# Kernel tuning notes

Measured on AMD Instinct MI355X. Metric: run time of the kernel, lower is better.

## Reference

```python
import jax, jax.numpy as jnp
import numpy as np

B, S, D, M, H, HD, V = 256, 128, 512, 150, 8, 64, 10000
LN_EPS = 1e-5

def layer_norm(x, g, b):
    mu = jnp.mean(x, axis=-1, keepdims=True)
    var = jnp.mean((x - mu) ** 2, axis=-1, keepdims=True)
    return (x - mu) * jax.lax.rsqrt(var + LN_EPS) * g + b

def setup_inputs() -> dict:
    key = jax.random.key(0)
    ks = jax.random.split(key, 20)
    s = 0.02
    return {
        'x': jax.random.randint(ks[0], (B, S), 0, V),
        'emb': jax.random.normal(ks[1], (V, D)) * s,
        'W1': jax.random.normal(ks[2], (M, D, D)) * s,   # [mode, out, in]
        'b1': jnp.zeros((M, D)),
        'ln1_g': jnp.ones((M, D)),
        'ln1_b': jnp.zeros((M, D)),
        'W2': jax.random.normal(ks[3], (M, D, D)) * s,
        'b2': jnp.zeros((M, D)),
        'dbias': jax.random.normal(ks[4], (M, D)) * 0.01,
        'in_proj_w': jax.random.normal(ks[5], (3 * D, D)) * s,
        'in_proj_b': jnp.zeros((3 * D,)),
        'out_proj_w': jax.random.normal(ks[6], (D, D)) * s,
        'out_proj_b': jnp.zeros((D,)),
        'norm_g': jnp.ones((D,)),
        'norm_b': jnp.zeros((D,)),
        'dec_w1': jax.random.normal(ks[7], (D // 2, D)) * s,
        'dec_b1': jnp.zeros((D // 2,)),
        'dec_w2': jax.random.normal(ks[8], (V, D // 2)) * s,
        'dec_b2': jnp.zeros((V,)),
    }

def reference(x, emb, W1, b1, ln1_g, ln1_b, W2, b2, dbias,
              in_proj_w, in_proj_b, out_proj_w, out_proj_b,
              norm_g, norm_b, dec_w1, dec_b1, dec_w2, dec_b2):
    # shared embedding: [B,S] -> [B,D]
    e = jnp.take(emb, x, axis=0).mean(axis=1)
    # 150 mode heads as grouped GEMMs: Linear -> LN -> ReLU -> Linear + bias
    h = jnp.einsum('bd,mod->bmo', e, W1) + b1                    # [B,M,D]
    h = layer_norm(h, ln1_g, ln1_b)
    h = jax.nn.relu(h)                                            # dropout = identity (eval)
    mode_out = jnp.einsum('bmd,mod->bmo', h, W2) + b2 + dbias     # [B,M,D]
    # cross-mode self-attention (torch MultiheadAttention, batch_first)
    qkv = mode_out @ in_proj_w.T + in_proj_b                      # [B,M,3D]
    q, k, v = jnp.split(qkv, 3, axis=-1)
    q = q.reshape(B, M, H, HD); k = k.reshape(B, M, H, HD); v = v.reshape(B, M, H, HD)
    scores = jnp.einsum('bqhd,bkhd->bhqk', q, k) / np.sqrt(HD)
    attn = jax.nn.softmax(scores, axis=-1)
    o = jnp.einsum('bhqk,bkhd->bqhd', attn, v).reshape(B, M, D)
    attended = o @ out_proj_w.T + out_proj_b                      # [B,M,D]
    # gating mask: active_modes=None -> all ones, so gated == attended
    agg = layer_norm(attended.sum(axis=1), norm_g, norm_b)        # [B,D]
    # decoder: Linear -> ReLU -> Linear
    dec = jax.nn.relu(agg @ dec_w1.T + dec_b1)
    return dec @ dec_w2.T + dec_b2                                # [B,V]
```

## Files before the change

kernel.cpp:

```cpp
#include <hip/hip_runtime.h>

typedef __attribute__((ext_vector_type(8))) short s16x8;
typedef __attribute__((ext_vector_type(8))) unsigned short u16x8;
typedef __attribute__((ext_vector_type(4))) float f32x4;

#define LN_EPS 1e-5f

__device__ inline float bf2f(unsigned short u) {
    union { unsigned int i; float f; } x; x.i = ((unsigned int)u) << 16; return x.f;
}
__device__ inline unsigned short f2bf(float f) {
    unsigned int u = __builtin_bit_cast(unsigned int, f);
    u += 0x7FFFu + ((u >> 16) & 1u);
    return (unsigned short)(u >> 16);
}
__device__ inline unsigned int cvt_pk_bf16(float lo, float hi) {
    unsigned int r;
    asm("v_cvt_pk_bf16_f32 %0, %1, %2" : "=v"(r) : "v"(lo), "v"(hi));
    return r;
}
typedef __attribute__((address_space(1))) const unsigned int as1_u32;
typedef __attribute__((address_space(3))) unsigned int as3_u32;
__device__ inline void gl2lds16(const void* g, void* l) {
    __builtin_amdgcn_global_load_lds((as1_u32*)g, (as3_u32*)l, 16, 0, 0);
}

template<int K, bool RELU, bool F32OUT>
__global__ __launch_bounds__(256, 3) void gemm_k32_kernel(
    const unsigned short* __restrict__ A,
    const float* __restrict__ W,
    const float* __restrict__ bias1,
    const float* __restrict__ bias2,
    float bias_scale,
    void* __restrict__ Cv,
    int N, int gx, int gy,
    size_t strideA_mode, size_t lda,
    size_t strideW_mode, size_t strideB_mode,
    size_t strideC_mode, size_t ldc)
{
    constexpr int NSTEP = K / 32;

    const int nwg = gridDim.x, wgid = blockIdx.x;
    const int q8 = nwg >> 3, r8 = nwg & 7;
    const int xcd = wgid & 7, sub = wgid >> 3;
    int p = (xcd < r8 ? xcd * (q8 + 1) : r8 * (q8 + 1) + (xcd - r8) * q8) + sub;
    const int bx = p % gx; p /= gx;
    const int by = p % gy;
    const int bz = p / gy;
    const int n0 = bx * 128, r0 = by * 128;

    __shared__ __align__(16) unsigned char lds[2][24576];

    const int tid = threadIdx.x, lane = tid & 63, wid = tid >> 6;
    const int fr = lane & 15, ks = lane >> 4;
    const int wr = (wid >> 1) * 64, wc = (wid & 1) * 64;

    const int Ia0 = (wid * 2 + 0) * 64 + lane;
    const int Ia1 = (wid * 2 + 1) * 64 + lane;
    const int ar0 = Ia0 >> 2, ac0 = (Ia0 & 3) ^ (ar0 & 3);
    const int ar1 = Ia1 >> 2, ac1 = (Ia1 & 3) ^ (ar1 & 3);
    const unsigned char* Aslab = (const unsigned char*)(A + (size_t)bz * strideA_mode);
    const unsigned char* aSrc0 = Aslab + (size_t)(r0 + ar0) * lda * 2 + ac0 * 16;
    const unsigned char* aSrc1 = Aslab + (size_t)(r0 + ar1) * lda * 2 + ac1 * 16;

    const unsigned char* Wslab = (const unsigned char*)(W + (size_t)bz * strideW_mode);
    const unsigned char* bSrc[4];
#pragma unroll
    for (int j = 0; j < 4; ++j) {
        const int I = (wid * 4 + j) * 64 + lane;
        const int brow = I >> 3, bcp = I & 7;
        const int bcl = bcp ^ (brow & 7);
        const int growb = min(n0 + brow, N - 1);
        bSrc[j] = Wslab + (size_t)growb * K * 4 + bcl * 16;
    }

    f32x4 acc[4][4];
#pragma unroll
    for (int i = 0; i < 4; ++i)
#pragma unroll
        for (int j = 0; j < 4; ++j)
#pragma unroll
            for (int r = 0; r < 4; ++r) acc[i][j][r] = 0.f;

    auto stage = [&](int buf, int t) {
        gl2lds16(aSrc0 + (size_t)t * 64, &lds[buf][(wid * 2 + 0) * 1024]);
        gl2lds16(aSrc1 + (size_t)t * 64, &lds[buf][(wid * 2 + 1) * 1024]);
#pragma unroll
        for (int j = 0; j < 4; ++j)
            gl2lds16(bSrc[j] + (size_t)t * 128, &lds[buf][8192 + (wid * 4 + j) * 1024]);
    };

    auto compute = [&](int buf) {
        const unsigned char* Ab = &lds[buf][0];
        const unsigned char* Bb = &lds[buf][8192];
        s16x8 af[4];
#pragma unroll
        for (int mi = 0; mi < 4; ++mi)
            af[mi] = *(const s16x8*)(Ab + (wr + mi * 16 + fr) * 64 + ((ks ^ (fr & 3)) << 4));
        s16x8 bfr[4];
#pragma unroll
        for (int ni = 0; ni < 4; ++ni) {
            const int brow = wc + ni * 16 + fr;
            const float4 v0 = *(const float4*)(Bb + brow * 128 + (((2 * ks + 0) ^ (fr & 7)) << 4));
            const float4 v1 = *(const float4*)(Bb + brow * 128 + (((2 * ks + 1) ^ (fr & 7)) << 4));
            union { unsigned int u[4]; s16x8 s; } r;
            r.u[0] = cvt_pk_bf16(v0.x, v0.y);
            r.u[1] = cvt_pk_bf16(v0.z, v0.w);
            r.u[2] = cvt_pk_bf16(v1.x, v1.y);
            r.u[3] = cvt_pk_bf16(v1.z, v1.w);
            bfr[ni] = r.s;
        }
#pragma unroll
        for (int mi = 0; mi < 4; ++mi)
#pragma unroll
            for (int ni = 0; ni < 4; ++ni)
                acc[mi][ni] = __builtin_amdgcn_mfma_f32_16x16x32_bf16(af[mi], bfr[ni], acc[mi][ni], 0, 0, 0);
    };

    stage(0, 0);
    __syncthreads();

    for (int t = 0; t < NSTEP; t += 2) {
        stage(1, t + 1);
        compute(0);
        __syncthreads();
        if (t + 2 < NSTEP) stage(0, t + 2);
        compute(1);
        __syncthreads();
    }

    if (!F32OUT) {
        unsigned short* Cl = (unsigned short*)&lds[0][0];
#pragma unroll
        for (int ni = 0; ni < 4; ++ni) {
            const int col = n0 + wc + ni * 16 + fr;
            float bsum = 0.f;
            if (bias1) bsum += bias_scale * bias1[(size_t)bz * strideB_mode + col];
            if (bias2) bsum += bias2[(size_t)bz * strideB_mode + col];
#pragma unroll
            for (int mi = 0; mi < 4; ++mi)
#pragma unroll
                for (int r = 0; r < 4; ++r) {
                    float v = acc[mi][ni][r] + bsum;
                    if (RELU) v = fmaxf(v, 0.f);
                    Cl[(wr + mi * 16 + ks * 4 + r) * 128 + wc + ni * 16 + fr] = f2bf(v);
                }
        }
        __syncthreads();
        unsigned short* Cg = (unsigned short*)Cv + (size_t)bz * strideC_mode;
#pragma unroll
        for (int it = 0; it < 8; ++it) {
            const int c = it * 256 + tid;
            const int row = c >> 4, ch = c & 15;
            u16x8 v = *(const u16x8*)(&Cl[row * 128 + ch * 8]);
            *(u16x8*)(Cg + (size_t)(r0 + row) * ldc + n0 + ch * 8) = v;
        }
    } else {
#pragma unroll
        for (int ni = 0; ni < 4; ++ni) {
            const int col = n0 + wc + ni * 16 + fr;
            if (col < N) {
                float bsum = 0.f;
                if (bias1) bsum += bias_scale * bias1[(size_t)bz * strideB_mode + col];
                if (bias2) bsum += bias2[(size_t)bz * strideB_mode + col];
#pragma unroll
                for (int mi = 0; mi < 4; ++mi)
#pragma unroll
                    for (int r = 0; r < 4; ++r) {
                        const int row = r0 + wr + mi * 16 + ks * 4 + r;
                        float v = acc[mi][ni][r] + bsum;
                        if (RELU) v = fmaxf(v, 0.f);
                        ((float*)Cv)[(size_t)bz * strideC_mode + (size_t)row * ldc + col] = v;
                    }
            }
        }
    }
}

__global__ __launch_bounds__(512) void embed_kernel(
    const int* __restrict__ x, const float* __restrict__ emb,
    unsigned short* __restrict__ e)
{
    const int b = blockIdx.x;
    __shared__ int xs[128];
    const int tid = threadIdx.x;
    if (tid < 128) xs[tid] = x[b * 128 + tid];
    __syncthreads();
    float s = 0.f;
    for (int i = 0; i < 128; ++i) s += emb[(size_t)xs[i] * 512 + tid];
    e[(size_t)b * 512 + tid] = f2bf(s * (1.f / 128.f));
}

template<bool RELU>
__global__ __launch_bounds__(256) void ln_kernel(
    const unsigned short* __restrict__ X,
    const float* __restrict__ G,
    const float* __restrict__ Bt,
    unsigned short* __restrict__ Y,
    int M)
{
    const int row = blockIdx.x;
    const int m = row % M;
    const unsigned short* xr = X + (size_t)row * 512;
    unsigned short* yr = Y + (size_t)row * 512;
    const int tid = threadIdx.x;
    const float x0 = bf2f(xr[tid]), x1 = bf2f(xr[tid + 256]);
    float s = x0 + x1, q = x0 * x0 + x1 * x1;
#pragma unroll
    for (int off = 32; off; off >>= 1) {
        s += __shfl_xor(s, off);
        q += __shfl_xor(q, off);
    }
    __shared__ float red[4][2];
    const int wid = tid >> 6, lane = tid & 63;
    if (lane == 0) { red[wid][0] = s; red[wid][1] = q; }
    __syncthreads();
    s = red[0][0] + red[1][0] + red[2][0] + red[3][0];
    q = red[0][1] + red[1][1] + red[2][1] + red[3][1];
    const float mu = s * (1.f / 512.f);
    const float var = q * (1.f / 512.f) - mu * mu;
    const float rstd = rsqrtf(var + LN_EPS);
    const float* g = G + (size_t)m * 512;
    const float* bt = Bt + (size_t)m * 512;
    float y0 = (x0 - mu) * rstd * g[tid] + bt[tid];
    float y1 = (x1 - mu) * rstd * g[tid + 256] + bt[tid + 256];
    if (RELU) { y0 = fmaxf(y0, 0.f); y1 = fmaxf(y1, 0.f); }
    yr[tid] = f2bf(y0);
    yr[tid + 256] = f2bf(y1);
}

#define KP 72
#define VP 168
__global__ __launch_bounds__(256) void attn_mfma_kernel(
    const unsigned short* __restrict__ qkv, unsigned short* __restrict__ o_att)
{
    const int b = blockIdx.x >> 3, h = blockIdx.x & 7;
    __shared__ __align__(16) unsigned short k_s[160 * KP];
    __shared__ __align__(16) unsigned short v_t[64 * VP];
    __shared__ __align__(16) unsigned short p_s[4][16 * VP];
    const int tid = threadIdx.x, lane = tid & 63, wid = tid >> 6;
    const int fr = lane & 15, ks = lane >> 4;
    const size_t base = (size_t)b * (150 * 1536) + h * 64;

    for (int idx = tid; idx < 160 * 8; idx += 256) {
        const int r = idx >> 3, c8 = (idx & 7) * 8;
        u16x8 v;
        if (r < 150) v = *(const u16x8*)(qkv + base + (size_t)r * 1536 + 512 + c8);
        else {
#pragma unroll
            for (int j = 0; j < 8; ++j) v[j] = 0;
        }
        *(u16x8*)(&k_s[r * KP + c8]) = v;
    }
    for (int idx = tid; idx < 160 * 8; idx += 256) {
        const int c8 = idx / 160, r = idx - c8 * 160;
        u16x8 v;
        if (r < 150) v = *(const u16x8*)(qkv + base + (size_t)r * 1536 + 1024 + c8 * 8);
        else {
#pragma unroll
            for (int j = 0; j < 8; ++j) v[j] = 0;
        }
#pragma unroll
        for (int j = 0; j < 8; ++j) v_t[(c8 * 8 + j) * VP + r] = v[j];
    }
    __syncthreads();

    unsigned short* pw = &p_s[wid][0];

    for (int qt = wid; qt < 10; qt += 4) {
        const int qr = (qt * 16 + fr < 150) ? qt * 16 + fr : 149;
        const unsigned short* qp = qkv + base + (size_t)qr * 1536;
        s16x8 qa0 = *(const s16x8*)(qp + ks * 8);
        s16x8 qa1 = *(const s16x8*)(qp + 32 + ks * 8);

        f32x4 acc[10];
#pragma unroll
        for (int t = 0; t < 10; ++t)
#pragma unroll
            for (int r = 0; r < 4; ++r) acc[t][r] = 0.f;
#pragma unroll
        for (int t = 0; t < 10; ++t) {
            s16x8 kb0 = *(const s16x8*)(&k_s[(t * 16 + fr) * KP + ks * 8]);
            s16x8 kb1 = *(const s16x8*)(&k_s[(t * 16 + fr) * KP + 32 + ks * 8]);
            acc[t] = __builtin_amdgcn_mfma_f32_16x16x32_bf16(qa0, kb0, acc[t], 0, 0, 0);
            acc[t] = __builtin_amdgcn_mfma_f32_16x16x32_bf16(qa1, kb1, acc[t], 0, 0, 0);
        }

        const bool v9 = (fr < 6);
        float inv[4];
#pragma unroll
        for (int i = 0; i < 4; ++i) {
            float m = -1e30f;
#pragma unroll
            for (int t = 0; t < 9; ++t) m = fmaxf(m, acc[t][i]);
            if (v9) m = fmaxf(m, acc[9][i]);
#pragma unroll
            for (int off = 1; off < 16; off <<= 1) m = fmaxf(m, __shfl_xor(m, off));
            float s = 0.f;
#pragma unroll
            for (int t = 0; t < 10; ++t) {
                float e = 0.f;
                if (t < 9 || v9) e = __expf(0.125f * (acc[t][i] - m));
                s += e;
                pw[(ks * 4 + i) * VP + t * 16 + fr] = f2bf(e);
            }
#pragma unroll
            for (int off = 1; off < 16; off <<= 1) s += __shfl_xor(s, off);
            inv[i] = 1.f / s;
        }

        f32x4 o[4];
#pragma unroll
        for (int dt = 0; dt < 4; ++dt)
#pragma unroll
            for (int r = 0; r < 4; ++r) o[dt][r] = 0.f;
#pragma unroll
        for (int kc = 0; kc < 5; ++kc) {
            s16x8 pa = *(const s16x8*)(&pw[fr * VP + kc * 32 + ks * 8]);
#pragma unroll
            for (int dt = 0; dt < 4; ++dt) {
                s16x8 vb = *(const s16x8*)(&v_t[(dt * 16 + fr) * VP + kc * 32 + ks * 8]);
                o[dt] = __builtin_amdgcn_mfma_f32_16x16x32_bf16(pa, vb, o[dt], 0, 0, 0);
            }
        }

#pragma unroll
        for (int dt = 0; dt < 4; ++dt) {
            const int d = h * 64 + dt * 16 + fr;
#pragma unroll
            for (int i = 0; i < 4; ++i) {
                const int q = qt * 16 + ks * 4 + i;
                if (q < 150)
                    o_att[((size_t)(b * 150 + q)) * 512 + d] = f2bf(o[dt][i] * inv[i]);
            }
        }
    }
}

__global__ __launch_bounds__(512) void osum_kernel(
    const unsigned short* __restrict__ o_att, unsigned short* __restrict__ osum)
{
    const int b = blockIdx.x, tid = threadIdx.x;
    float s = 0.f;
    const unsigned short* p = o_att + (size_t)b * 150 * 512 + tid;
    for (int mm = 0; mm < 150; ++mm) s += bf2f(p[(size_t)mm * 512]);
    osum[(size_t)b * 512 + tid] = f2bf(s);
}

extern "C" void kernel_launch(void* const* d_in, const int* in_sizes, int n_in,
                              void* d_out, int out_size, void* d_ws, size_t ws_size,
                              hipStream_t stream)
{
    (void)in_sizes; (void)n_in; (void)out_size; (void)ws_size;

    const int*   x          = (const int*)d_in[0];
    const float* emb        = (const float*)d_in[1];
    const float* W1         = (const float*)d_in[2];
    const float* b1         = (const float*)d_in[3];
    const float* ln1_g      = (const float*)d_in[4];
    const float* ln1_b      = (const float*)d_in[5];
    const float* W2         = (const float*)d_in[6];
    const float* b2         = (const float*)d_in[7];
    const float* dbias      = (const float*)d_in[8];
    const float* in_proj_w  = (const float*)d_in[9];
    const float* in_proj_b  = (const float*)d_in[10];
    const float* out_proj_w = (const float*)d_in[11];
    const float* out_proj_b = (const float*)d_in[12];
    const float* norm_g     = (const float*)d_in[13];
    const float* norm_b     = (const float*)d_in[14];
    const float* dec_w1     = (const float*)d_in[15];
    const float* dec_b1     = (const float*)d_in[16];
    const float* dec_w2     = (const float*)d_in[17];
    const float* dec_b2     = (const float*)d_in[18];

    char* ws = (char*)d_ws;
    unsigned short* e_bf  = (unsigned short*)(ws + 0x0);
    unsigned short* osum  = (unsigned short*)(ws + 0x40000);
    unsigned short* att1  = (unsigned short*)(ws + 0x80000);
    unsigned short* agg   = (unsigned short*)(ws + 0xC0000);
    unsigned short* dec1  = (unsigned short*)(ws + 0x100000);
    unsigned short* h1    = (unsigned short*)(ws + 0x200000);
    unsigned short* mo    = (unsigned short*)(ws + 0x2800000);
    unsigned short* qkvf  = (unsigned short*)(ws + 0x4E00000);
    unsigned short* o_att = h1;

    embed_kernel<<<256, 512, 0, stream>>>(x, emb, e_bf);

    gemm_k32_kernel<512, false, false><<<4 * 2 * 150, 256, 0, stream>>>(
        e_bf, W1, b1, nullptr, 1.f, h1,
        512, 4, 2,
        (size_t)0, 512, (size_t)512 * 512, 512, 512, 76800);

    ln_kernel<true><<<38400, 256, 0, stream>>>(h1, ln1_g, ln1_b, h1, 150);

    gemm_k32_kernel<512, false, false><<<4 * 2 * 150, 256, 0, stream>>>(
        h1, W2, b2, dbias, 1.f, mo,
        512, 4, 2,
        (size_t)512, 76800, (size_t)512 * 512, 512, 512, 76800);

    gemm_k32_kernel<512, false, false><<<12 * 300, 256, 0, stream>>>(
        mo, in_proj_w, in_proj_b, nullptr, 1.f, qkvf,
        1536, 12, 300,
        (size_t)0, 512, (size_t)0, 0, 0, 1536);

    attn_mfma_kernel<<<2048, 256, 0, stream>>>(qkvf, o_att);

    osum_kernel<<<256, 512, 0, stream>>>(o_att, osum);

    gemm_k32_kernel<512, false, false><<<4 * 2, 256, 0, stream>>>(
        osum, out_proj_w, out_proj_b, nullptr, 150.f, att1,
        512, 4, 2,
        (size_t)0, 512, (size_t)0, 0, 0, 512);

    ln_kernel<false><<<256, 256, 0, stream>>>(att1, norm_g, norm_b, agg, 1);

    gemm_k32_kernel<512, true, false><<<2 * 2, 256, 0, stream>>>(
        agg, dec_w1, dec_b1, nullptr, 1.f, dec1,
        256, 2, 2,
        (size_t)0, 512, (size_t)0, 0, 0, 256);

    gemm_k32_kernel<256, false, true><<<79 * 2, 256, 0, stream>>>(
        dec1, dec_w2, dec_b2, nullptr, 1.f, d_out,
        10000, 79, 2,
        (size_t)0, 256, (size_t)0, 0, 0, 10000);
}
```

Measured before the change: 407.4 us.

## Pre-convert weights to bf16 and chunk QKV GEMM with attention per batch slice

Adds a conversion kernel that turns every fp32 weight matrix into bf16 in the workspace before use. The GEMM kernel now streams bf16 weights, which halves weight traffic and LDS per stage, removes the in-loop fp32-to-bf16 conversions and allows occupancy 4. Separately, the QKV projection and attention now run in four batch chunks of 64 so the QKV buffer stays small and likely cache-resident. The trade-off is an extra full read and write pass over the 150-mode W1/W2 weights on every call, plus more kernel launches.

```diff
diff --git a/kernel.cpp b/kernel.cpp
--- a/kernel.cpp
+++ b/kernel.cpp
@@ -25,10 +25,27 @@
     __builtin_amdgcn_global_load_lds((as1_u32*)g, (as3_u32*)l, 16, 0, 0);
 }
 
+__global__ __launch_bounds__(256) void cvt_bf16_kernel(
+    const float* __restrict__ in, unsigned short* __restrict__ out, int n8)
+{
+    int i = blockIdx.x * 256 + threadIdx.x;
+    const int stride = gridDim.x * 256;
+    for (; i < n8; i += stride) {
+        const float4 a = ((const float4*)in)[2 * i];
+        const float4 b = ((const float4*)in)[2 * i + 1];
+        union { unsigned int u[4]; u16x8 v; } r;
+        r.u[0] = cvt_pk_bf16(a.x, a.y);
+        r.u[1] = cvt_pk_bf16(a.z, a.w);
+        r.u[2] = cvt_pk_bf16(b.x, b.y);
+        r.u[3] = cvt_pk_bf16(b.z, b.w);
+        ((u16x8*)out)[i] = r.v;
+    }
+}
+
 template<int K, bool RELU, bool F32OUT>
-__global__ __launch_bounds__(256, 3) void gemm_k32_kernel(
+__global__ __launch_bounds__(256, 4) void gemm_bf_kernel(
     const unsigned short* __restrict__ A,
-    const float* __restrict__ W,
+    const unsigned short* __restrict__ Wb,
     const float* __restrict__ bias1,
     const float* __restrict__ bias2,
     float bias_scale,
@@ -49,7 +66,7 @@
     const int bz = p / gy;
     const int n0 = bx * 128, r0 = by * 128;
 
-    __shared__ __align__(16) unsigned char lds[2][24576];
+    __shared__ __align__(16) unsigned char lds[2][16384];
 
     const int tid = threadIdx.x, lane = tid & 63, wid = tid >> 6;
     const int fr = lane & 15, ks = lane >> 4;
@@ -62,17 +79,10 @@
     const unsigned char* Aslab = (const unsigned char*)(A + (size_t)bz * strideA_mode);
     const unsigned char* aSrc0 = Aslab + (size_t)(r0 + ar0) * lda * 2 + ac0 * 16;
     const unsigned char* aSrc1 = Aslab + (size_t)(r0 + ar1) * lda * 2 + ac1 * 16;
-
-    const unsigned char* Wslab = (const unsigned char*)(W + (size_t)bz * strideW_mode);
-    const unsigned char* bSrc[4];
-#pragma unroll
-    for (int j = 0; j < 4; ++j) {
-        const int I = (wid * 4 + j) * 64 + lane;
-        const int brow = I >> 3, bcp = I & 7;
-        const int bcl = bcp ^ (brow & 7);
-        const int growb = min(n0 + brow, N - 1);
-        bSrc[j] = Wslab + (size_t)growb * K * 4 + bcl * 16;
-    }
+    const unsigned char* Wslab = (const unsigned char*)(Wb + (size_t)bz * strideW_mode);
+    const int br0 = min(n0 + ar0, N - 1), br1 = min(n0 + ar1, N - 1);
+    const unsigned char* bSrc0 = Wslab + (size_t)br0 * K * 2 + ac0 * 16;
+    const unsigned char* bSrc1 = Wslab + (size_t)br1 * K * 2 + ac1 * 16;
 
     f32x4 acc[4][4];
 #pragma unroll
@@ -85,31 +95,21 @@
     auto stage = [&](int buf, int t) {
         gl2lds16(aSrc0 + (size_t)t * 64, &lds[buf][(wid * 2 + 0) * 1024]);
         gl2lds16(aSrc1 + (size_t)t * 64, &lds[buf][(wid * 2 + 1) * 1024]);
-#pragma unroll
-        for (int j = 0; j < 4; ++j)
-            gl2lds16(bSrc[j] + (size_t)t * 128, &lds[buf][8192 + (wid * 4 + j) * 1024]);
+        gl2lds16(bSrc0 + (size_t)t * 64, &lds[buf][8192 + (wid * 2 + 0) * 1024]);
+        gl2lds16(bSrc1 + (size_t)t * 64, &lds[buf][8192 + (wid * 2 + 1) * 1024]);
     };
 
     auto compute = [&](int buf) {
         const unsigned char* Ab = &lds[buf][0];
         const unsigned char* Bb = &lds[buf][8192];
-        s16x8 af[4];
+        const int co = (ks ^ (fr & 3)) << 4;
+        s16x8 af[4], bfr[4];
 #pragma unroll
         for (int mi = 0; mi < 4; ++mi)
-            af[mi] = *(const s16x8*)(Ab + (wr + mi * 16 + fr) * 64 + ((ks ^ (fr & 3)) << 4));
-        s16x8 bfr[4];
-#pragma unroll
-        for (int ni = 0; ni < 4; ++ni) {
-            const int brow = wc + ni * 16 + fr;
-            const float4 v0 = *(const float4*)(Bb + brow * 128 + (((2 * ks + 0) ^ (fr & 7)) << 4));
-            const float4 v1 = *(const float4*)(Bb + brow * 128 + (((2 * ks + 1) ^ (fr & 7)) << 4));
-            union { unsigned int u[4]; s16x8 s; } r;
-            r.u[0] = cvt_pk_bf16(v0.x, v0.y);
-            r.u[1] = cvt_pk_bf16(v0.z, v0.w);
-            r.u[2] = cvt_pk_bf16(v1.x, v1.y);
-            r.u[3] = cvt_pk_bf16(v1.z, v1.w);
-            bfr[ni] = r.s;
-        }
+            af[mi] = *(const s16x8*)(Ab + (wr + mi * 16 + fr) * 64 + co);
+#pragma unroll
+        for (int ni = 0; ni < 4; ++ni)
+            bfr[ni] = *(const s16x8*)(Bb + (wc + ni * 16 + fr) * 64 + co);
 #pragma unroll
         for (int mi = 0; mi < 4; ++mi)
 #pragma unroll
@@ -232,15 +232,16 @@
 #define KP 72
 #define VP 168
 __global__ __launch_bounds__(256) void attn_mfma_kernel(
-    const unsigned short* __restrict__ qkv, unsigned short* __restrict__ o_att)
-{
-    const int b = blockIdx.x >> 3, h = blockIdx.x & 7;
+    const unsigned short* __restrict__ qkv, unsigned short* __restrict__ o_att,
+    int b0)
+{
+    const int bl = blockIdx.x >> 3, h = blockIdx.x & 7;
     __shared__ __align__(16) unsigned short k_s[160 * KP];
     __shared__ __align__(16) unsigned short v_t[64 * VP];
     __shared__ __align__(16) unsigned short p_s[4][16 * VP];
     const int tid = threadIdx.x, lane = tid & 63, wid = tid >> 6;
     const int fr = lane & 15, ks = lane >> 4;
-    const size_t base = (size_t)b * (150 * 1536) + h * 64;
+    const size_t base = (size_t)bl * (150 * 1536) + h * 64;
 
     for (int idx = tid; idx < 160 * 8; idx += 256) {
         const int r = idx >> 3, c8 = (idx & 7) * 8;
@@ -331,7 +332,7 @@
             for (int i = 0; i < 4; ++i) {
                 const int q = qt * 16 + ks * 4 + i;
                 if (q < 150)
-                    o_att[((size_t)(b * 150 + q)) * 512 + d] = f2bf(o[dt][i] * inv[i]);
+                    o_att[((size_t)((b0 + bl) * 150 + q)) * 512 + d] = f2bf(o[dt][i] * inv[i]);
             }
         }
     }
@@ -381,46 +382,61 @@
     unsigned short* dec1  = (unsigned short*)(ws + 0x100000);
     unsigned short* h1    = (unsigned short*)(ws + 0x200000);
     unsigned short* mo    = (unsigned short*)(ws + 0x2800000);
-    unsigned short* qkvf  = (unsigned short*)(ws + 0x4E00000);
+    unsigned short* qkvb  = (unsigned short*)(ws + 0x4E00000);
+    unsigned short* Wbf   = (unsigned short*)(ws + 0x6B00000);
+    unsigned short* ipwbf = (unsigned short*)(ws + 0xB600000);
+    unsigned short* opwbf = (unsigned short*)(ws + 0xB780000);
+    unsigned short* dw1bf = (unsigned short*)(ws + 0xB800000);
+    unsigned short* dw2bf = (unsigned short*)(ws + 0xB840000);
     unsigned short* o_att = h1;
 
     embed_kernel<<<256, 512, 0, stream>>>(x, emb, e_bf);
 
-    gemm_k32_kernel<512, false, false><<<4 * 2 * 150, 256, 0, stream>>>(
-        e_bf, W1, b1, nullptr, 1.f, h1,
+    cvt_bf16_kernel<<<384, 256, 0, stream>>>(in_proj_w, ipwbf, 1536 * 512 / 8);
+    cvt_bf16_kernel<<<128, 256, 0, stream>>>(out_proj_w, opwbf, 512 * 512 / 8);
+    cvt_bf16_kernel<<<64, 256, 0, stream>>>(dec_w1, dw1bf, 256 * 512 / 8);
+    cvt_bf16_kernel<<<1280, 256, 0, stream>>>(dec_w2, dw2bf, 10000 * 256 / 8);
+
+    cvt_bf16_kernel<<<2048, 256, 0, stream>>>(W1, Wbf, 150 * 512 * 512 / 8);
+
+    gemm_bf_kernel<512, false, false><<<4 * 2 * 150, 256, 0, stream>>>(
+        e_bf, Wbf, b1, nullptr, 1.f, h1,
         512, 4, 2,
         (size_t)0, 512, (size_t)512 * 512, 512, 512, 76800);
 
     ln_kernel<true><<<38400, 256, 0, stream>>>(h1, ln1_g, ln1_b, h1, 150);
 
-    gemm_k32_kernel<512, false, false><<<4 * 2 * 150, 256, 0, stream>>>(
-        h1, W2, b2, dbias, 1.f, mo,
+    cvt_bf16_kernel<<<2048, 256, 0, stream>>>(W2, Wbf, 150 * 512 * 512 / 8);
+
+    gemm_bf_kernel<512, false, false><<<4 * 2 * 150, 256, 0, stream>>>(
+        h1, Wbf, b2, dbias, 1.f, mo,
         512, 4, 2,
         (size_t)512, 76800, (size_t)512 * 512, 512, 512, 76800);
 
-    gemm_k32_kernel<512, false, false><<<12 * 300, 256, 0, stream>>>(
-        mo, in_proj_w, in_proj_b, nullptr, 1.f, qkvf,
-        1536, 12, 300,
-        (size_t)0, 512, (size_t)0, 0, 0, 1536);
-
-    attn_mfma_kernel<<<2048, 256, 0, stream>>>(qkvf, o_att);
+    for (int c = 0; c < 4; ++c) {
+        gemm_bf_kernel<512, false, false><<<12 * 75, 256, 0, stream>>>(
+            mo + (size_t)c * 64 * 76800, ipwbf, in_proj_b, nullptr, 1.f, qkvb,
+            1536, 12, 75,
+            (size_t)0, 512, (size_t)0, 0, 0, 1536);
+        attn_mfma_kernel<<<512, 256, 0, stream>>>(qkvb, o_att, c * 64);
+    }
 
     osum_kernel<<<256, 512, 0, stream>>>(o_att, osum);
 
-    gemm_k32_kernel<512, false, false><<<4 * 2, 256, 0, stream>>>(
-        osum, out_proj_w, out_proj_b, nullptr, 150.f, att1,
+    gemm_bf_kernel<512, false, false><<<4 * 2, 256, 0, stream>>>(
+        osum, opwbf, out_proj_b, nullptr, 150.f, att1,
         512, 4, 2,
         (size_t)0, 512, (size_t)0, 0, 0, 512);
 
     ln_kernel<false><<<256, 256, 0, stream>>>(att1, norm_g, norm_b, agg, 1);
 
-    gemm_k32_kernel<512, true, false><<<2 * 2, 256, 0, stream>>>(
-        agg, dec_w1, dec_b1, nullptr, 1.f, dec1,
+    gemm_bf_kernel<512, true, false><<<2 * 2, 256, 0, stream>>>(
+        agg, dw1bf, dec_b1, nullptr, 1.f, dec1,
         256, 2, 2,
         (size_t)0, 512, (size_t)0, 0, 0, 256);
 
-    gemm_k32_kernel<256, false, true><<<79 * 2, 256, 0, stream>>>(
-        dec1, dec_w2, dec_b2, nullptr, 1.f, d_out,
+    gemm_bf_kernel<256, false, true><<<79 * 2, 256, 0, stream>>>(
+        dec1, dw2bf, dec_b2, nullptr, 1.f, d_out,
         10000, 79, 2,
         (size_t)0, 256, (size_t)0, 0, 0, 10000);
 }
```

After: 419.1 us. +2.9%, slower.
